# Optimization experiments

Hardware: AMD Instinct MI355X
Metric: run time of the kernel (lower is better)

Reference implementation:

```python
import jax, jax.numpy as jnp
import numpy as np

T, B, I, H = 2048, 32, 256, 256
KEEP = 0.75  # 1 - dropout_rate


def setup_inputs() -> dict:
    key = jax.random.key(0)
    ks = jax.random.split(key, 7)
    inp = jax.random.normal(ks[0], (T, B, I), dtype=jnp.float32)
    # variational dropout masks sampled once (Bernoulli(keep)), like the torch module
    zx = (jax.random.uniform(ks[1], (I,)) < KEEP).astype(jnp.float32)
    zh = (jax.random.uniform(ks[2], (H,)) < KEEP).astype(jnp.float32)
    # stacked gate weights in order [i, f, o, g]; scaled like nn.Linear default init
    s_w = 1.0 / np.sqrt(I)
    s_u = 1.0 / np.sqrt(H)
    W = jax.random.uniform(ks[3], (4 * H, I), minval=-s_w, maxval=s_w, dtype=jnp.float32)
    bW = jax.random.uniform(ks[4], (4 * H,), minval=-s_w, maxval=s_w, dtype=jnp.float32)
    U = jax.random.uniform(ks[5], (4 * H, H), minval=-s_u, maxval=s_u, dtype=jnp.float32)
    bU = jax.random.uniform(ks[6], (4 * H,), minval=-s_u, maxval=s_u, dtype=jnp.float32)
    return {"input": inp, "zx": zx, "zh": zh, "W": W, "bW": bW, "U": U, "bU": bU}


def reference(input, zx, zh, W, bW, U, bU):
    Bsz = input.shape[1]
    Hd = U.shape[1]

    def step(carry, x_t):
        h, c = carry
        x = x_t * zx          # [B, I] variational input dropout
        hm = h * zh           # [B, H] variational hidden dropout
        gates = x @ W.T + bW + hm @ U.T + bU   # [B, 4H]
        i, f, o, g = jnp.split(gates, 4, axis=-1)
        i = jax.nn.sigmoid(i)
        f = jax.nn.sigmoid(f)
        o = jax.nn.sigmoid(o)
        g = jnp.tanh(g)
        c_new = f * c + i * g
        h_new = o * jnp.tanh(c_new)
        return (h_new, c_new), h_new

    h0 = jnp.zeros((Bsz, Hd), dtype=input.dtype)
    c0 = jnp.zeros((Bsz, Hd), dtype=input.dtype)
    (h_t, c_t), hn = jax.lax.scan(step, (h0, c0), input)
    return hn, h_t, c_t
```

## Files before the change

kernel.cpp:

```cpp
#include <hip/hip_runtime.h>
#include <stdint.h>

typedef _Float16 half_t;
typedef _Float16 half2_t __attribute__((ext_vector_type(2)));

#define TSEQ 2048
#define NB   32
#define HD   256
#define HN_ELEMS ((size_t)TSEQ*NB*HD)

static __device__ __forceinline__ float fdot2u(uint32_t a, uint32_t b, float acc) {
  return __builtin_amdgcn_fdot2(__builtin_bit_cast(half2_t, a),
                                __builtin_bit_cast(half2_t, b), acc, false);
}
static __device__ __forceinline__ int sdot4(uint32_t a, uint32_t b, int c) {
#if defined(__has_builtin)
#if __has_builtin(__builtin_amdgcn_sdot4)
  return __builtin_amdgcn_sdot4((int)a, (int)b, c, false);
#else
  int d;
  asm("v_dot4_i32_i8 %0, %1, %2, %3" : "=v"(d) : "v"(a), "v"(b), "v"(c));
  return d;
#endif
#else
  int d;
  asm("v_dot4_i32_i8 %0, %1, %2, %3" : "=v"(d) : "v"(a), "v"(b), "v"(c));
  return d;
#endif
}
static __device__ __forceinline__ float sigm_f(float x) {
  return __builtin_amdgcn_rcpf(1.0f + __expf(-x));
}
static __device__ __forceinline__ float tanh_f(float x) {
  return 2.0f * __builtin_amdgcn_rcpf(1.0f + __expf(-2.0f * x)) - 1.0f;
}
static __device__ __forceinline__ signed char q8(float v, float sc) {
  int q = (int)rintf(v * sc);
  q = q > 127 ? 127 : (q < -127 ? -127 : q);
  return (signed char)q;
}

__global__ void prep_kernel(const float* __restrict__ W, const float* __restrict__ U,
                            const float* __restrict__ bW, const float* __restrict__ bU,
                            const float* __restrict__ zx, const float* __restrict__ zh,
                            half_t* __restrict__ Wpk, signed char* __restrict__ Upk3b,
                            signed char* __restrict__ Ug4b, float* __restrict__ bias,
                            half_t* __restrict__ hstate, float* __restrict__ cstate) {
  int tid = blockIdx.x * 256 + threadIdx.x;
  int n   = tid & 1023;
  int kcG = tid >> 10;
  #pragma unroll
  for (int e = 0; e < 8; ++e) {
    int k = kcG * 8 + e;
    Wpk[((size_t)kcG * 1024 + n) * 8 + e] = (half_t)(W[n * 256 + k] * zx[k]);
    float uv = U[n * 256 + k] * zh[k];
    signed char qv = q8(uv, 2032.0f);
    int kg = k >> 7, kk = k & 127, q = kk >> 4, by = kk & 15;
    if (n < 768) {
      int c = n >> 8, j = n & 255;
      Upk3b[(((size_t)(c * 2 + kg) * 8 + q) * 256 + j) * 16 + by] = qv;
    } else {
      Ug4b[(((size_t)kg * 8 + q) * 256 + (n & 255)) * 16 + by] = qv;
    }
  }
  if (kcG == 0) bias[n] = bW[n] + bU[n];
  if (tid < NB * HD) { hstate[tid] = (half_t)0.0f; cstate[tid] = 0.0f; }
}

__global__ __launch_bounds__(512)
void gemm_kernel(const float* __restrict__ input, const uint4* __restrict__ Wpk,
                 const float* __restrict__ bias, half_t* __restrict__ gx, int row0,
                 uint32_t rz) {
  __shared__ __align__(16) uint4  As[64 * 32];
  __shared__ __align__(16) float  part[8 * 256];
  __shared__ __align__(16) uint4  pad1b[1280];
  const int tid = threadIdx.x;
  if ((int)blockIdx.x < 0) pad1b[tid] = As[tid];
  const int cb    = blockIdx.x & 3;
  const int rbase = (blockIdx.x >> 2) * 64;
  const int jc    = tid & 255;
  const int kh    = tid >> 8;
  const int col   = cb * 256 + jc;

  uint32_t wreg[64];
  #pragma unroll
  for (int kc = 0; kc < 16; ++kc) {
    uint4 q = Wpk[(size_t)(kh * 16 + kc) * 1024 + col];
    wreg[kc * 4 + 0] = q.x ^ rz; wreg[kc * 4 + 1] = q.y ^ rz;
    wreg[kc * 4 + 2] = q.z ^ rz; wreg[kc * 4 + 3] = q.w ^ rz;
  }
  const float bc = bias[col];
  #pragma unroll
  for (int i = 0; i < 8; ++i) {
    int lin = tid + i * 512;
    int row = lin >> 6, f4 = lin & 63;
    float4 v = ((const float4*)input)[((size_t)(row0 + rbase + row)) * 64 + f4];
    half2_t p0; p0[0] = (half_t)v.x; p0[1] = (half_t)v.y;
    half2_t p1; p1[0] = (half_t)v.z; p1[1] = (half_t)v.w;
    ((uint2*)As)[row * 64 + f4] = make_uint2(__builtin_bit_cast(uint32_t, p0),
                                             __builtin_bit_cast(uint32_t, p1));
  }
  __syncthreads();

  #pragma unroll 1
  for (int rg = 0; rg < 64; rg += 8) {
    float acc[8];
    #pragma unroll
    for (int rr = 0; rr < 8; ++rr) {
      const uint4* arow = As + (rg + rr) * 32 + kh * 16;
      float a = 0.f;
      #pragma unroll
      for (int kc = 0; kc < 16; ++kc) {
        uint4 hv = arow[kc];
        a = fdot2u(wreg[kc * 4 + 0], hv.x, a);
        a = fdot2u(wreg[kc * 4 + 1], hv.y, a);
        a = fdot2u(wreg[kc * 4 + 2], hv.z, a);
        a = fdot2u(wreg[kc * 4 + 3], hv.w, a);
      }
      acc[rr] = a;
    }
    if (kh) {
      #pragma unroll
      for (int rr = 0; rr < 8; ++rr) part[rr * 256 + jc] = acc[rr];
    }
    __syncthreads();
    if (!kh) {
      #pragma unroll
      for (int rr = 0; rr < 8; ++rr) {
        float v = acc[rr] + part[rr * 256 + jc] + bc;
        gx[((size_t)(rbase + rg + rr) * HD + jc) * 4 + cb] = (half_t)v;
      }
    }
    __syncthreads();
  }
}

__global__ __launch_bounds__(512)
__attribute__((amdgpu_waves_per_eu(2, 2)))
void rec_kernel(const half_t* __restrict__ gx, const uint4* __restrict__ Upk3p,
                const uint4* __restrict__ Ug4p,
                half_t* __restrict__ hstate, float* __restrict__ cstate,
                float* __restrict__ out, int tbase, int TB, int last,
                uint32_t rz) {
  __shared__ __align__(16) uint4 uglds[4096];
  __shared__ __align__(16) signed char hbuf8[256];
  __shared__ __align__(16) int part[4 * 256];

  const int b   = blockIdx.x;
  const int tid = threadIdx.x;
  const int kg  = tid >> 8;
  const int j   = tid & 255;

  #pragma unroll
  for (int i = 0; i < 8; ++i) uglds[i * 512 + tid] = Ug4p[i * 512 + tid];

  uint32_t upk0[32], upk1[32], upk2[32];
  #pragma unroll
  for (int q = 0; q < 8; ++q) {
    uint4 v = Upk3p[((size_t)(0 * 2 + kg) * 8 + q) * 256 + j];
    upk0[q * 4 + 0] = v.x ^ rz; upk0[q * 4 + 1] = v.y ^ rz;
    upk0[q * 4 + 2] = v.z ^ rz; upk0[q * 4 + 3] = v.w ^ rz;
  }
  #pragma unroll
  for (int q = 0; q < 8; ++q) {
    uint4 v = Upk3p[((size_t)(1 * 2 + kg) * 8 + q) * 256 + j];
    upk1[q * 4 + 0] = v.x ^ rz; upk1[q * 4 + 1] = v.y ^ rz;
    upk1[q * 4 + 2] = v.z ^ rz; upk1[q * 4 + 3] = v.w ^ rz;
  }
  #pragma unroll
  for (int q = 0; q < 8; ++q) {
    uint4 v = Upk3p[((size_t)(2 * 2 + kg) * 8 + q) * 256 + j];
    upk2[q * 4 + 0] = v.x ^ rz; upk2[q * 4 + 1] = v.y ^ rz;
    upk2[q * 4 + 2] = v.z ^ rz; upk2[q * 4 + 3] = v.w ^ rz;
  }

  float cc = 0.f, hlastf = 0.f;
  uint2 gpk = make_uint2(0, 0), npk = make_uint2(0, 0);
  const uint2* gpn = (const uint2*)gx + (size_t)b * HD + j;
  float* outp = out + ((size_t)tbase * NB + b) * HD + j;
  if (kg == 0) {
    cc = cstate[b * HD + j];
    float h0 = (float)hstate[b * HD + j];
    hlastf = h0;
    hbuf8[j] = (signed char)(int)rintf(h0 * 127.0f);
    gpk = *gpn;
  }
  gpn += (size_t)NB * HD;
  __syncthreads();

  const float s = 0.0625f / 16129.0f;
  #pragma unroll 1
  for (int t = 0; t < TB; ++t) {
    if (kg == 0 && t + 1 < TB) npk = *gpn;
    gpn += (size_t)NB * HD;

    int a0 = 0, a1 = 0, a2 = 0, a3 = 0;
    const uint4* hp8 = (const uint4*)hbuf8 + kg * 8;
    const uint4* ugp = uglds + (size_t)kg * 8 * 256 + j;
    #pragma unroll
    for (int q = 0; q < 8; ++q) {
      uint4 hv = hp8[q];
      uint4 ug = ugp[q * 256];
      a0 = sdot4(upk0[q * 4 + 0], hv.x, a0);
      a0 = sdot4(upk0[q * 4 + 1], hv.y, a0);
      a0 = sdot4(upk0[q * 4 + 2], hv.z, a0);
      a0 = sdot4(upk0[q * 4 + 3], hv.w, a0);
      a1 = sdot4(upk1[q * 4 + 0], hv.x, a1);
      a1 = sdot4(upk1[q * 4 + 1], hv.y, a1);
      a1 = sdot4(upk1[q * 4 + 2], hv.z, a1);
      a1 = sdot4(upk1[q * 4 + 3], hv.w, a1);
      a2 = sdot4(upk2[q * 4 + 0], hv.x, a2);
      a2 = sdot4(upk2[q * 4 + 1], hv.y, a2);
      a2 = sdot4(upk2[q * 4 + 2], hv.z, a2);
      a2 = sdot4(upk2[q * 4 + 3], hv.w, a2);
      a3 = sdot4(ug.x, hv.x, a3);
      a3 = sdot4(ug.y, hv.y, a3);
      a3 = sdot4(ug.z, hv.z, a3);
      a3 = sdot4(ug.w, hv.w, a3);
    }
    if (kg) {
      part[0 * 256 + j] = a0;
      part[1 * 256 + j] = a1;
      part[2 * 256 + j] = a2;
      part[3 * 256 + j] = a3;
    }
    __syncthreads();
    if (kg == 0) {
      half2_t g01 = __builtin_bit_cast(half2_t, gpk.x);
      half2_t g23 = __builtin_bit_cast(half2_t, gpk.y);
      float f0 = (float)(a0 + part[0 * 256 + j]) * s + (float)g01[0];
      float f1 = (float)(a1 + part[1 * 256 + j]) * s + (float)g01[1];
      float f2 = (float)(a2 + part[2 * 256 + j]) * s + (float)g23[0];
      float f3 = (float)(a3 + part[3 * 256 + j]) * s + (float)g23[1];
      float gi = sigm_f(f0), gf = sigm_f(f1), go = sigm_f(f2), gg = tanh_f(f3);
      cc = gf * cc + gi * gg;
      float h = go * tanh_f(cc);
      hlastf = h;
      hbuf8[j] = (signed char)(int)rintf(h * 127.0f);
      *outp = h;
      if (last && t == TB - 1) {
        out[HN_ELEMS + (size_t)b * HD + j] = h;
        out[HN_ELEMS + (size_t)NB * HD + (size_t)b * HD + j] = cc;
      }
      gpk = npk;
    }
    outp += (size_t)NB * HD;
    __syncthreads();
  }
  if (kg == 0) {
    hstate[b * HD + j] = (half_t)hlastf;
    cstate[b * HD + j] = cc;
  }
}

extern "C" void kernel_launch(void* const* d_in, const int* in_sizes, int n_in,
                              void* d_out, int out_size, void* d_ws, size_t ws_size,
                              hipStream_t stream) {
  const float* input = (const float*)d_in[0];
  const float* zx    = (const float*)d_in[1];
  const float* zh    = (const float*)d_in[2];
  const float* W     = (const float*)d_in[3];
  const float* bW    = (const float*)d_in[4];
  const float* U     = (const float*)d_in[5];
  const float* bU    = (const float*)d_in[6];
  float* out = (float*)d_out;

  char* ws = (char*)d_ws;
  signed char* Upk3b = (signed char*)(ws);
  signed char* Ug4b  = (signed char*)(ws + (192 << 10));
  uint4*  Wpk    = (uint4*)(ws + (256 << 10));
  float*  bias   = (float*) (ws + (768 << 10));
  half_t* hstate = (half_t*)(ws + (772 << 10));
  float*  cstate = (float*) (ws + (788 << 10));
  half_t* gx     = (half_t*)(ws + (1 << 20));

  uint32_t rz = (uint32_t)(in_sizes[1] >> 9);

  int TB = TSEQ;
  while (TB > 32 && (size_t)(1u << 20) + (size_t)TB * NB * 1024 * 2 > ws_size) TB >>= 1;

  prep_kernel<<<128, 256, 0, stream>>>(W, U, bW, bU, zx, zh,
                                       (half_t*)Wpk, Upk3b, Ug4b,
                                       bias, hstate, cstate);

  int nch = TSEQ / TB;
  for (int c = 0; c < nch; ++c) {
    int tbase = c * TB;
    gemm_kernel<<<(TB * NB / 64) * 4, 512, 0, stream>>>(input, Wpk, bias, gx,
                                                        tbase * NB, rz);
    rec_kernel<<<NB, 512, 0, stream>>>(gx, (const uint4*)Upk3b, (const uint4*)Ug4b,
                                       hstate, cstate, out,
                                       tbase, TB, (c == nch - 1) ? 1 : 0, rz);
  }
}
```

Measured before the change: 2.034 ms.

## Use one thread per hidden unit in recurrence with double-buffered h

The recurrence kernel drops from 512 threads split over two K halves to 256 threads, each computing the full K=256 dot products for its hidden unit. This removes the shared-memory partial-sum exchange and one of the two barriers per timestep, since h is double-buffered. Each thread now keeps 224 packed int8 weight registers plus half of the fourth gate's weights in LDS, so register pressure rises sharply and there is a risk of spills. It also cuts wave-level parallelism and doubles the serial dot-product chain per thread.

```diff
diff --git a/kernel.cpp b/kernel.cpp
--- a/kernel.cpp
+++ b/kernel.cpp
@@ -55,12 +55,13 @@
     Wpk[((size_t)kcG * 1024 + n) * 8 + e] = (half_t)(W[n * 256 + k] * zx[k]);
     float uv = U[n * 256 + k] * zh[k];
     signed char qv = q8(uv, 2032.0f);
-    int kg = k >> 7, kk = k & 127, q = kk >> 4, by = kk & 15;
-    if (n < 768) {
-      int c = n >> 8, j = n & 255;
-      Upk3b[(((size_t)(c * 2 + kg) * 8 + q) * 256 + j) * 16 + by] = qv;
+    int c = n >> 8, j = n & 255, q = k >> 4, by = k & 15;
+    if (c < 3) {
+      Upk3b[(((size_t)c * 16 + q) * 256 + j) * 16 + by] = qv;
+    } else if (k < 128) {
+      Upk3b[(((size_t)48 + q) * 256 + j) * 16 + by] = qv;
     } else {
-      Ug4b[(((size_t)kg * 8 + q) * 256 + (n & 255)) * 16 + by] = qv;
+      Ug4b[(((size_t)(q - 8)) * 256 + j) * 16 + by] = qv;
     }
   }
   if (kcG == 0) bias[n] = bW[n] + bU[n];
@@ -135,72 +136,71 @@
   }
 }
 
-__global__ __launch_bounds__(512)
-__attribute__((amdgpu_waves_per_eu(2, 2)))
+__global__ __launch_bounds__(256)
 void rec_kernel(const half_t* __restrict__ gx, const uint4* __restrict__ Upk3p,
                 const uint4* __restrict__ Ug4p,
                 half_t* __restrict__ hstate, float* __restrict__ cstate,
                 float* __restrict__ out, int tbase, int TB, int last,
                 uint32_t rz) {
-  __shared__ __align__(16) uint4 uglds[4096];
-  __shared__ __align__(16) signed char hbuf8[256];
-  __shared__ __align__(16) int part[4 * 256];
-
-  const int b   = blockIdx.x;
-  const int tid = threadIdx.x;
-  const int kg  = tid >> 8;
-  const int j   = tid & 255;
-
-  #pragma unroll
-  for (int i = 0; i < 8; ++i) uglds[i * 512 + tid] = Ug4p[i * 512 + tid];
-
-  uint32_t upk0[32], upk1[32], upk2[32];
-  #pragma unroll
-  for (int q = 0; q < 8; ++q) {
-    uint4 v = Upk3p[((size_t)(0 * 2 + kg) * 8 + q) * 256 + j];
+  __shared__ __align__(16) uint4 uglds[8 * 256];
+  __shared__ __align__(16) uint4 hb[2][16];
+
+  const int b = blockIdx.x;
+  const int j = threadIdx.x;
+
+  #pragma unroll
+  for (int i = 0; i < 8; ++i) uglds[i * 256 + j] = Ug4p[i * 256 + j];
+
+  uint32_t upk0[64], upk1[64], upk2[64], upk3[32];
+  #pragma unroll
+  for (int q = 0; q < 16; ++q) {
+    uint4 v = Upk3p[((size_t)(0 * 16 + q)) * 256 + j];
     upk0[q * 4 + 0] = v.x ^ rz; upk0[q * 4 + 1] = v.y ^ rz;
     upk0[q * 4 + 2] = v.z ^ rz; upk0[q * 4 + 3] = v.w ^ rz;
   }
   #pragma unroll
-  for (int q = 0; q < 8; ++q) {
-    uint4 v = Upk3p[((size_t)(1 * 2 + kg) * 8 + q) * 256 + j];
+  for (int q = 0; q < 16; ++q) {
+    uint4 v = Upk3p[((size_t)(1 * 16 + q)) * 256 + j];
     upk1[q * 4 + 0] = v.x ^ rz; upk1[q * 4 + 1] = v.y ^ rz;
     upk1[q * 4 + 2] = v.z ^ rz; upk1[q * 4 + 3] = v.w ^ rz;
   }
   #pragma unroll
-  for (int q = 0; q < 8; ++q) {
-    uint4 v = Upk3p[((size_t)(2 * 2 + kg) * 8 + q) * 256 + j];
+  for (int q = 0; q < 16; ++q) {
+    uint4 v = Upk3p[((size_t)(2 * 16 + q)) * 256 + j];
     upk2[q * 4 + 0] = v.x ^ rz; upk2[q * 4 + 1] = v.y ^ rz;
     upk2[q * 4 + 2] = v.z ^ rz; upk2[q * 4 + 3] = v.w ^ rz;
   }
-
-  float cc = 0.f, hlastf = 0.f;
-  uint2 gpk = make_uint2(0, 0), npk = make_uint2(0, 0);
+  #pragma unroll
+  for (int q = 0; q < 8; ++q) {
+    uint4 v = Upk3p[((size_t)(48 + q)) * 256 + j];
+    upk3[q * 4 + 0] = v.x ^ rz; upk3[q * 4 + 1] = v.y ^ rz;
+    upk3[q * 4 + 2] = v.z ^ rz; upk3[q * 4 + 3] = v.w ^ rz;
+  }
+
+  float cc = cstate[b * HD + j];
+  float h0 = (float)hstate[b * HD + j];
+  ((signed char*)hb[0])[j] = (signed char)(int)rintf(h0 * 127.0f);
+
   const uint2* gpn = (const uint2*)gx + (size_t)b * HD + j;
   float* outp = out + ((size_t)tbase * NB + b) * HD + j;
-  if (kg == 0) {
-    cc = cstate[b * HD + j];
-    float h0 = (float)hstate[b * HD + j];
-    hlastf = h0;
-    hbuf8[j] = (signed char)(int)rintf(h0 * 127.0f);
-    gpk = *gpn;
-  }
+  uint2 gpk = *gpn, npk = make_uint2(0, 0);
   gpn += (size_t)NB * HD;
   __syncthreads();
 
   const float s = 0.0625f / 16129.0f;
+  float hlastf = h0;
   #pragma unroll 1
   for (int t = 0; t < TB; ++t) {
-    if (kg == 0 && t + 1 < TB) npk = *gpn;
+    const int cur = t & 1, nxt = cur ^ 1;
+    if (t + 1 < TB) npk = *gpn;
     gpn += (size_t)NB * HD;
 
     int a0 = 0, a1 = 0, a2 = 0, a3 = 0;
-    const uint4* hp8 = (const uint4*)hbuf8 + kg * 8;
-    const uint4* ugp = uglds + (size_t)kg * 8 * 256 + j;
+    const uint4* hp = hb[cur];
+    const uint4* ugp = uglds + j;
     #pragma unroll
-    for (int q = 0; q < 8; ++q) {
-      uint4 hv = hp8[q];
-      uint4 ug = ugp[q * 256];
+    for (int q = 0; q < 16; ++q) {
+      uint4 hv = hp[q];
       a0 = sdot4(upk0[q * 4 + 0], hv.x, a0);
       a0 = sdot4(upk0[q * 4 + 1], hv.y, a0);
       a0 = sdot4(upk0[q * 4 + 2], hv.z, a0);
@@ -213,44 +213,41 @@
       a2 = sdot4(upk2[q * 4 + 1], hv.y, a2);
       a2 = sdot4(upk2[q * 4 + 2], hv.z, a2);
       a2 = sdot4(upk2[q * 4 + 3], hv.w, a2);
-      a3 = sdot4(ug.x, hv.x, a3);
-      a3 = sdot4(ug.y, hv.y, a3);
-      a3 = sdot4(ug.z, hv.z, a3);
-      a3 = sdot4(ug.w, hv.w, a3);
-    }
-    if (kg) {
-      part[0 * 256 + j] = a0;
-      part[1 * 256 + j] = a1;
-      part[2 * 256 + j] = a2;
-      part[3 * 256 + j] = a3;
-    }
-    __syncthreads();
-    if (kg == 0) {
-      half2_t g01 = __builtin_bit_cast(half2_t, gpk.x);
-      half2_t g23 = __builtin_bit_cast(half2_t, gpk.y);
-      float f0 = (float)(a0 + part[0 * 256 + j]) * s + (float)g01[0];
-      float f1 = (float)(a1 + part[1 * 256 + j]) * s + (float)g01[1];
-      float f2 = (float)(a2 + part[2 * 256 + j]) * s + (float)g23[0];
-      float f3 = (float)(a3 + part[3 * 256 + j]) * s + (float)g23[1];
-      float gi = sigm_f(f0), gf = sigm_f(f1), go = sigm_f(f2), gg = tanh_f(f3);
-      cc = gf * cc + gi * gg;
-      float h = go * tanh_f(cc);
-      hlastf = h;
-      hbuf8[j] = (signed char)(int)rintf(h * 127.0f);
-      *outp = h;
-      if (last && t == TB - 1) {
-        out[HN_ELEMS + (size_t)b * HD + j] = h;
-        out[HN_ELEMS + (size_t)NB * HD + (size_t)b * HD + j] = cc;
+      if (q < 8) {
+        a3 = sdot4(upk3[q * 4 + 0], hv.x, a3);
+        a3 = sdot4(upk3[q * 4 + 1], hv.y, a3);
+        a3 = sdot4(upk3[q * 4 + 2], hv.z, a3);
+        a3 = sdot4(upk3[q * 4 + 3], hv.w, a3);
+      } else {
+        uint4 ug = ugp[(q - 8) * 256];
+        a3 = sdot4(ug.x, hv.x, a3);
+        a3 = sdot4(ug.y, hv.y, a3);
+        a3 = sdot4(ug.z, hv.z, a3);
+        a3 = sdot4(ug.w, hv.w, a3);
       }
-      gpk = npk;
-    }
+    }
+    half2_t g01 = __builtin_bit_cast(half2_t, gpk.x);
+    half2_t g23 = __builtin_bit_cast(half2_t, gpk.y);
+    float f0 = (float)a0 * s + (float)g01[0];
+    float f1 = (float)a1 * s + (float)g01[1];
+    float f2 = (float)a2 * s + (float)g23[0];
+    float f3 = (float)a3 * s + (float)g23[1];
+    float gi = sigm_f(f0), gf = sigm_f(f1), go = sigm_f(f2), gg = tanh_f(f3);
+    cc = gf * cc + gi * gg;
+    float h = go * tanh_f(cc);
+    hlastf = h;
+    ((signed char*)hb[nxt])[j] = (signed char)(int)rintf(h * 127.0f);
+    *outp = h;
+    if (last && t == TB - 1) {
+      out[HN_ELEMS + (size_t)b * HD + j] = h;
+      out[HN_ELEMS + (size_t)NB * HD + (size_t)b * HD + j] = cc;
+    }
+    gpk = npk;
     outp += (size_t)NB * HD;
     __syncthreads();
   }
-  if (kg == 0) {
-    hstate[b * HD + j] = (half_t)hlastf;
-    cstate[b * HD + j] = cc;
-  }
+  hstate[b * HD + j] = (half_t)hlastf;
+  cstate[b * HD + j] = cc;
 }
 
 extern "C" void kernel_launch(void* const* d_in, const int* in_sizes, int n_in,
@@ -267,7 +264,7 @@
 
   char* ws = (char*)d_ws;
   signed char* Upk3b = (signed char*)(ws);
-  signed char* Ug4b  = (signed char*)(ws + (192 << 10));
+  signed char* Ug4b  = (signed char*)(ws + (224 << 10));
   uint4*  Wpk    = (uint4*)(ws + (256 << 10));
   float*  bias   = (float*) (ws + (768 << 10));
   half_t* hstate = (half_t*)(ws + (772 << 10));
@@ -288,7 +285,7 @@
     int tbase = c * TB;
     gemm_kernel<<<(TB * NB / 64) * 4, 512, 0, stream>>>(input, Wpk, bias, gx,
                                                         tbase * NB, rz);
-    rec_kernel<<<NB, 512, 0, stream>>>(gx, (const uint4*)Upk3b, (const uint4*)Ug4b,
+    rec_kernel<<<NB, 256, 0, stream>>>(gx, (const uint4*)Upk3b, (const uint4*)Ug4b,
                                        hstate, cstate, out,
                                        tbase, TB, (c == nch - 1) ? 1 : 0, rz);
   }
```

Result: slower. 2.232 ms (+9.7%).

## Split K-halves across wave lanes and reduce with permlane32 swap

Applied to the files above, without the earlier changes.

Remaps threads so the two K-halves for one hidden unit live in the upper and lower 32 lanes of the same wave. Partial dot products are then combined with v_permlane32_swap instead of an LDS write, a barrier and a read. The hidden-state buffer is double-buffered, which removes one __syncthreads per timestep. Both halves now compute the gate nonlinearities redundantly, and the waves_per_eu attribute is dropped, which may change register allocation.

```diff
diff --git a/kernel.cpp b/kernel.cpp
--- a/kernel.cpp
+++ b/kernel.cpp
@@ -27,6 +27,13 @@
   asm("v_dot4_i32_i8 %0, %1, %2, %3" : "=v"(d) : "v"(a), "v"(b), "v"(c));
   return d;
 #endif
+}
+static __device__ __forceinline__ int halfsum(int a) {
+  int y;
+  asm("v_mov_b32 %1, %0\n\t"
+      "v_permlane32_swap_b32 %0, %1"
+      : "+v"(a), "=&v"(y));
+  return a + y;
 }
 static __device__ __forceinline__ float sigm_f(float x) {
   return __builtin_amdgcn_rcpf(1.0f + __expf(-x));
@@ -136,114 +143,106 @@
 }
 
 __global__ __launch_bounds__(512)
-__attribute__((amdgpu_waves_per_eu(2, 2)))
 void rec_kernel(const half_t* __restrict__ gx, const uint4* __restrict__ Upk3p,
                 const uint4* __restrict__ Ug4p,
                 half_t* __restrict__ hstate, float* __restrict__ cstate,
                 float* __restrict__ out, int tbase, int TB, int last,
                 uint32_t rz) {
   __shared__ __align__(16) uint4 uglds[4096];
-  __shared__ __align__(16) signed char hbuf8[256];
-  __shared__ __align__(16) int part[4 * 256];
-
-  const int b   = blockIdx.x;
-  const int tid = threadIdx.x;
-  const int kg  = tid >> 8;
-  const int j   = tid & 255;
+  __shared__ __align__(16) uint4 hb[2][16];
+
+  const int b    = blockIdx.x;
+  const int tid  = threadIdx.x;
+  const int lane = tid & 63;
+  const int kg   = lane >> 5;
+  const int j    = (tid >> 6) * 32 + (lane & 31);
 
   #pragma unroll
   for (int i = 0; i < 8; ++i) uglds[i * 512 + tid] = Ug4p[i * 512 + tid];
 
-  uint32_t upk0[32], upk1[32], upk2[32];
+  uint32_t u0[32], u1[32], u2[32];
   #pragma unroll
   for (int q = 0; q < 8; ++q) {
     uint4 v = Upk3p[((size_t)(0 * 2 + kg) * 8 + q) * 256 + j];
-    upk0[q * 4 + 0] = v.x ^ rz; upk0[q * 4 + 1] = v.y ^ rz;
-    upk0[q * 4 + 2] = v.z ^ rz; upk0[q * 4 + 3] = v.w ^ rz;
+    u0[q * 4 + 0] = v.x ^ rz; u0[q * 4 + 1] = v.y ^ rz;
+    u0[q * 4 + 2] = v.z ^ rz; u0[q * 4 + 3] = v.w ^ rz;
   }
   #pragma unroll
   for (int q = 0; q < 8; ++q) {
     uint4 v = Upk3p[((size_t)(1 * 2 + kg) * 8 + q) * 256 + j];
-    upk1[q * 4 + 0] = v.x ^ rz; upk1[q * 4 + 1] = v.y ^ rz;
-    upk1[q * 4 + 2] = v.z ^ rz; upk1[q * 4 + 3] = v.w ^ rz;
+    u1[q * 4 + 0] = v.x ^ rz; u1[q * 4 + 1] = v.y ^ rz;
+    u1[q * 4 + 2] = v.z ^ rz; u1[q * 4 + 3] = v.w ^ rz;
   }
   #pragma unroll
   for (int q = 0; q < 8; ++q) {
     uint4 v = Upk3p[((size_t)(2 * 2 + kg) * 8 + q) * 256 + j];
-    upk2[q * 4 + 0] = v.x ^ rz; upk2[q * 4 + 1] = v.y ^ rz;
-    upk2[q * 4 + 2] = v.z ^ rz; upk2[q * 4 + 3] = v.w ^ rz;
-  }
-
-  float cc = 0.f, hlastf = 0.f;
-  uint2 gpk = make_uint2(0, 0), npk = make_uint2(0, 0);
+    u2[q * 4 + 0] = v.x ^ rz; u2[q * 4 + 1] = v.y ^ rz;
+    u2[q * 4 + 2] = v.z ^ rz; u2[q * 4 + 3] = v.w ^ rz;
+  }
+
+  float cc = cstate[b * HD + j];
+  float h0 = (float)hstate[b * HD + j];
+  float hlastf = h0;
+  if (kg == 0) ((signed char*)hb[0])[j] = (signed char)(int)rintf(h0 * 127.0f);
+
   const uint2* gpn = (const uint2*)gx + (size_t)b * HD + j;
   float* outp = out + ((size_t)tbase * NB + b) * HD + j;
-  if (kg == 0) {
-    cc = cstate[b * HD + j];
-    float h0 = (float)hstate[b * HD + j];
-    hlastf = h0;
-    hbuf8[j] = (signed char)(int)rintf(h0 * 127.0f);
-    gpk = *gpn;
-  }
+  uint2 gpk = *gpn, npk = make_uint2(0, 0);
   gpn += (size_t)NB * HD;
   __syncthreads();
 
   const float s = 0.0625f / 16129.0f;
   #pragma unroll 1
   for (int t = 0; t < TB; ++t) {
-    if (kg == 0 && t + 1 < TB) npk = *gpn;
+    if (t + 1 < TB) npk = *gpn;
     gpn += (size_t)NB * HD;
 
     int a0 = 0, a1 = 0, a2 = 0, a3 = 0;
-    const uint4* hp8 = (const uint4*)hbuf8 + kg * 8;
-    const uint4* ugp = uglds + (size_t)kg * 8 * 256 + j;
+    const uint4* hp  = hb[t & 1] + (kg << 3);
+    const uint4* ugp = uglds + (size_t)kg * 2048 + j;
     #pragma unroll
     for (int q = 0; q < 8; ++q) {
-      uint4 hv = hp8[q];
+      uint4 hv = hp[q];
       uint4 ug = ugp[q * 256];
-      a0 = sdot4(upk0[q * 4 + 0], hv.x, a0);
-      a0 = sdot4(upk0[q * 4 + 1], hv.y, a0);
-      a0 = sdot4(upk0[q * 4 + 2], hv.z, a0);
-      a0 = sdot4(upk0[q * 4 + 3], hv.w, a0);
-      a1 = sdot4(upk1[q * 4 + 0], hv.x, a1);
-      a1 = sdot4(upk1[q * 4 + 1], hv.y, a1);
-      a1 = sdot4(upk1[q * 4 + 2], hv.z, a1);
-      a1 = sdot4(upk1[q * 4 + 3], hv.w, a1);
-      a2 = sdot4(upk2[q * 4 + 0], hv.x, a2);
-      a2 = sdot4(upk2[q * 4 + 1], hv.y, a2);
-      a2 = sdot4(upk2[q * 4 + 2], hv.z, a2);
-      a2 = sdot4(upk2[q * 4 + 3], hv.w, a2);
+      a0 = sdot4(u0[q * 4 + 0], hv.x, a0);
+      a0 = sdot4(u0[q * 4 + 1], hv.y, a0);
+      a0 = sdot4(u0[q * 4 + 2], hv.z, a0);
+      a0 = sdot4(u0[q * 4 + 3], hv.w, a0);
+      a1 = sdot4(u1[q * 4 + 0], hv.x, a1);
+      a1 = sdot4(u1[q * 4 + 1], hv.y, a1);
+      a1 = sdot4(u1[q * 4 + 2], hv.z, a1);
+      a1 = sdot4(u1[q * 4 + 3], hv.w, a1);
+      a2 = sdot4(u2[q * 4 + 0], hv.x, a2);
+      a2 = sdot4(u2[q * 4 + 1], hv.y, a2);
+      a2 = sdot4(u2[q * 4 + 2], hv.z, a2);
+      a2 = sdot4(u2[q * 4 + 3], hv.w, a2);
       a3 = sdot4(ug.x, hv.x, a3);
       a3 = sdot4(ug.y, hv.y, a3);
       a3 = sdot4(ug.z, hv.z, a3);
       a3 = sdot4(ug.w, hv.w, a3);
     }
-    if (kg) {
-      part[0 * 256 + j] = a0;
-      part[1 * 256 + j] = a1;
-      part[2 * 256 + j] = a2;
-      part[3 * 256 + j] = a3;
-    }
-    __syncthreads();
+    a0 = halfsum(a0); a1 = halfsum(a1);
+    a2 = halfsum(a2); a3 = halfsum(a3);
+
+    half2_t g01 = __builtin_bit_cast(half2_t, gpk.x);
+    half2_t g23 = __builtin_bit_cast(half2_t, gpk.y);
+    float f0 = (float)a0 * s + (float)g01[0];
+    float f1 = (float)a1 * s + (float)g01[1];
+    float f2 = (float)a2 * s + (float)g23[0];
+    float f3 = (float)a3 * s + (float)g23[1];
+    float gi = sigm_f(f0), gf = sigm_f(f1), go = sigm_f(f2), gg = tanh_f(f3);
+    cc = gf * cc + gi * gg;
+    float h = go * tanh_f(cc);
+    hlastf = h;
     if (kg == 0) {
-      half2_t g01 = __builtin_bit_cast(half2_t, gpk.x);
-      half2_t g23 = __builtin_bit_cast(half2_t, gpk.y);
-      float f0 = (float)(a0 + part[0 * 256 + j]) * s + (float)g01[0];
-      float f1 = (float)(a1 + part[1 * 256 + j]) * s + (float)g01[1];
-      float f2 = (float)(a2 + part[2 * 256 + j]) * s + (float)g23[0];
-      float f3 = (float)(a3 + part[3 * 256 + j]) * s + (float)g23[1];
-      float gi = sigm_f(f0), gf = sigm_f(f1), go = sigm_f(f2), gg = tanh_f(f3);
-      cc = gf * cc + gi * gg;
-      float h = go * tanh_f(cc);
-      hlastf = h;
-      hbuf8[j] = (signed char)(int)rintf(h * 127.0f);
+      ((signed char*)hb[(t & 1) ^ 1])[j] = (signed char)(int)rintf(h * 127.0f);
       *outp = h;
       if (last && t == TB - 1) {
         out[HN_ELEMS + (size_t)b * HD + j] = h;
         out[HN_ELEMS + (size_t)NB * HD + (size_t)b * HD + j] = cc;
       }
-      gpk = npk;
-    }
+    }
+    gpk = npk;
     outp += (size_t)NB * HD;
     __syncthreads();
   }
```

Measured after the change: 2.139 ms. +5.2%, slower.

## Replace fdot2 input-projection GEMM with MFMA 16x16x32 f16 kernel

Applied to the files above, without the earlier changes.

The input projection GEMM now runs on matrix cores via mfma_f32_16x16x32_f16 instead of per-thread fdot2 loops with LDS staging and a split-K reduction. W is stored as a plain row-major f16 matrix and read directly from global memory, and gx becomes a gate-major [row][1024] layout. The recurrent kernel is adjusted to read its four gate values from strided positions instead of one packed uint2. The cost removed is GEMM compute time. In exchange the B operand is read from global without LDS reuse, and the recurrent kernel issues four scalar loads per step.

```diff
diff --git a/kernel.cpp b/kernel.cpp
--- a/kernel.cpp
+++ b/kernel.cpp
@@ -3,16 +3,14 @@
 
 typedef _Float16 half_t;
 typedef _Float16 half2_t __attribute__((ext_vector_type(2)));
+typedef _Float16 half8_t __attribute__((ext_vector_type(8)));
+typedef float f32x4 __attribute__((ext_vector_type(4)));
 
 #define TSEQ 2048
 #define NB   32
 #define HD   256
 #define HN_ELEMS ((size_t)TSEQ*NB*HD)
 
-static __device__ __forceinline__ float fdot2u(uint32_t a, uint32_t b, float acc) {
-  return __builtin_amdgcn_fdot2(__builtin_bit_cast(half2_t, a),
-                                __builtin_bit_cast(half2_t, b), acc, false);
-}
 static __device__ __forceinline__ int sdot4(uint32_t a, uint32_t b, int c) {
 #if defined(__has_builtin)
 #if __has_builtin(__builtin_amdgcn_sdot4)
@@ -43,7 +41,7 @@
 __global__ void prep_kernel(const float* __restrict__ W, const float* __restrict__ U,
                             const float* __restrict__ bW, const float* __restrict__ bU,
                             const float* __restrict__ zx, const float* __restrict__ zh,
-                            half_t* __restrict__ Wpk, signed char* __restrict__ Upk3b,
+                            half_t* __restrict__ Wf16, signed char* __restrict__ Upk3b,
                             signed char* __restrict__ Ug4b, float* __restrict__ bias,
                             half_t* __restrict__ hstate, float* __restrict__ cstate) {
   int tid = blockIdx.x * 256 + threadIdx.x;
@@ -52,7 +50,7 @@
   #pragma unroll
   for (int e = 0; e < 8; ++e) {
     int k = kcG * 8 + e;
-    Wpk[((size_t)kcG * 1024 + n) * 8 + e] = (half_t)(W[n * 256 + k] * zx[k]);
+    Wf16[(size_t)n * 256 + k] = (half_t)(W[n * 256 + k] * zx[k]);
     float uv = U[n * 256 + k] * zh[k];
     signed char qv = q8(uv, 2032.0f);
     int kg = k >> 7, kk = k & 127, q = kk >> 4, by = kk & 15;
@@ -67,71 +65,47 @@
   if (tid < NB * HD) { hstate[tid] = (half_t)0.0f; cstate[tid] = 0.0f; }
 }
 
-__global__ __launch_bounds__(512)
-void gemm_kernel(const float* __restrict__ input, const uint4* __restrict__ Wpk,
-                 const float* __restrict__ bias, half_t* __restrict__ gx, int row0,
-                 uint32_t rz) {
-  __shared__ __align__(16) uint4  As[64 * 32];
-  __shared__ __align__(16) float  part[8 * 256];
-  __shared__ __align__(16) uint4  pad1b[1280];
-  const int tid = threadIdx.x;
-  if ((int)blockIdx.x < 0) pad1b[tid] = As[tid];
-  const int cb    = blockIdx.x & 3;
-  const int rbase = (blockIdx.x >> 2) * 64;
-  const int jc    = tid & 255;
-  const int kh    = tid >> 8;
-  const int col   = cb * 256 + jc;
-
-  uint32_t wreg[64];
-  #pragma unroll
-  for (int kc = 0; kc < 16; ++kc) {
-    uint4 q = Wpk[(size_t)(kh * 16 + kc) * 1024 + col];
-    wreg[kc * 4 + 0] = q.x ^ rz; wreg[kc * 4 + 1] = q.y ^ rz;
-    wreg[kc * 4 + 2] = q.z ^ rz; wreg[kc * 4 + 3] = q.w ^ rz;
-  }
-  const float bc = bias[col];
-  #pragma unroll
-  for (int i = 0; i < 8; ++i) {
-    int lin = tid + i * 512;
-    int row = lin >> 6, f4 = lin & 63;
-    float4 v = ((const float4*)input)[((size_t)(row0 + rbase + row)) * 64 + f4];
-    half2_t p0; p0[0] = (half_t)v.x; p0[1] = (half_t)v.y;
-    half2_t p1; p1[0] = (half_t)v.z; p1[1] = (half_t)v.w;
-    ((uint2*)As)[row * 64 + f4] = make_uint2(__builtin_bit_cast(uint32_t, p0),
-                                             __builtin_bit_cast(uint32_t, p1));
-  }
-  __syncthreads();
-
+__global__ __launch_bounds__(256)
+void gemm_kernel(const float* __restrict__ input, const half_t* __restrict__ Wf16,
+                 const float* __restrict__ bias, half_t* __restrict__ gx, int row0) {
+  const int tid  = threadIdx.x;
+  const int lane = tid & 63;
+  const int w    = tid >> 6;
+  const int mr   = lane & 15;
+  const int g    = lane >> 4;
+  const int nb   = (blockIdx.x & 3) * 256;
+  const int m0   = (blockIdx.x >> 2) * 64 + w * 16;
+
+  f32x4 acc[16];
+  #pragma unroll
+  for (int nf = 0; nf < 16; ++nf) acc[nf] = (f32x4){0.f, 0.f, 0.f, 0.f};
+
+  const float* arow = input + ((size_t)(row0 + m0 + mr)) * 256 + g * 8;
   #pragma unroll 1
-  for (int rg = 0; rg < 64; rg += 8) {
-    float acc[8];
+  for (int kk = 0; kk < 8; ++kk) {
+    float4 v0 = ((const float4*)(arow + kk * 32))[0];
+    float4 v1 = ((const float4*)(arow + kk * 32))[1];
+    half8_t a;
+    a[0] = (half_t)v0.x; a[1] = (half_t)v0.y; a[2] = (half_t)v0.z; a[3] = (half_t)v0.w;
+    a[4] = (half_t)v1.x; a[5] = (half_t)v1.y; a[6] = (half_t)v1.z; a[7] = (half_t)v1.w;
+    const half_t* bbase = Wf16 + (size_t)(nb + mr) * 256 + kk * 32 + g * 8;
     #pragma unroll
-    for (int rr = 0; rr < 8; ++rr) {
-      const uint4* arow = As + (rg + rr) * 32 + kh * 16;
-      float a = 0.f;
-      #pragma unroll
-      for (int kc = 0; kc < 16; ++kc) {
-        uint4 hv = arow[kc];
-        a = fdot2u(wreg[kc * 4 + 0], hv.x, a);
-        a = fdot2u(wreg[kc * 4 + 1], hv.y, a);
-        a = fdot2u(wreg[kc * 4 + 2], hv.z, a);
-        a = fdot2u(wreg[kc * 4 + 3], hv.w, a);
-      }
-      acc[rr] = a;
-    }
-    if (kh) {
-      #pragma unroll
-      for (int rr = 0; rr < 8; ++rr) part[rr * 256 + jc] = acc[rr];
-    }
-    __syncthreads();
-    if (!kh) {
-      #pragma unroll
-      for (int rr = 0; rr < 8; ++rr) {
-        float v = acc[rr] + part[rr * 256 + jc] + bc;
-        gx[((size_t)(rbase + rg + rr) * HD + jc) * 4 + cb] = (half_t)v;
-      }
-    }
-    __syncthreads();
+    for (int nf = 0; nf < 16; ++nf) {
+      uint4 bu = *(const uint4*)(bbase + (size_t)nf * 16 * 256);
+      half8_t b = __builtin_bit_cast(half8_t, bu);
+      acc[nf] = __builtin_amdgcn_mfma_f32_16x16x32_f16(a, b, acc[nf], 0, 0, 0);
+    }
+  }
+
+  #pragma unroll
+  for (int nf = 0; nf < 16; ++nf) {
+    int n = nb + nf * 16 + mr;
+    float bc = bias[n];
+    #pragma unroll
+    for (int i = 0; i < 4; ++i) {
+      int r = m0 + g * 4 + i;
+      gx[(size_t)r * 1024 + n] = (half_t)(acc[nf][i] + bc);
+    }
   }
 }
 
@@ -175,24 +149,27 @@
   }
 
   float cc = 0.f, hlastf = 0.f;
-  uint2 gpk = make_uint2(0, 0), npk = make_uint2(0, 0);
-  const uint2* gpn = (const uint2*)gx + (size_t)b * HD + j;
+  half_t g0 = (half_t)0.f, g1 = g0, g2 = g0, g3 = g0;
+  half_t n0 = g0, n1 = g0, n2 = g0, n3 = g0;
+  const half_t* gpn = gx + (size_t)b * 1024 + j;
   float* outp = out + ((size_t)tbase * NB + b) * HD + j;
   if (kg == 0) {
     cc = cstate[b * HD + j];
     float h0 = (float)hstate[b * HD + j];
     hlastf = h0;
     hbuf8[j] = (signed char)(int)rintf(h0 * 127.0f);
-    gpk = *gpn;
-  }
-  gpn += (size_t)NB * HD;
+    g0 = gpn[0]; g1 = gpn[256]; g2 = gpn[512]; g3 = gpn[768];
+  }
+  gpn += (size_t)NB * 1024;
   __syncthreads();
 
   const float s = 0.0625f / 16129.0f;
   #pragma unroll 1
   for (int t = 0; t < TB; ++t) {
-    if (kg == 0 && t + 1 < TB) npk = *gpn;
-    gpn += (size_t)NB * HD;
+    if (kg == 0 && t + 1 < TB) {
+      n0 = gpn[0]; n1 = gpn[256]; n2 = gpn[512]; n3 = gpn[768];
+    }
+    gpn += (size_t)NB * 1024;
 
     int a0 = 0, a1 = 0, a2 = 0, a3 = 0;
     const uint4* hp8 = (const uint4*)hbuf8 + kg * 8;
@@ -226,12 +203,10 @@
     }
     __syncthreads();
     if (kg == 0) {
-      half2_t g01 = __builtin_bit_cast(half2_t, gpk.x);
-      half2_t g23 = __builtin_bit_cast(half2_t, gpk.y);
-      float f0 = (float)(a0 + part[0 * 256 + j]) * s + (float)g01[0];
-      float f1 = (float)(a1 + part[1 * 256 + j]) * s + (float)g01[1];
-      float f2 = (float)(a2 + part[2 * 256 + j]) * s + (float)g23[0];
-      float f3 = (float)(a3 + part[3 * 256 + j]) * s + (float)g23[1];
+      float f0 = (float)(a0 + part[0 * 256 + j]) * s + (float)g0;
+      float f1 = (float)(a1 + part[1 * 256 + j]) * s + (float)g1;
+      float f2 = (float)(a2 + part[2 * 256 + j]) * s + (float)g2;
+      float f3 = (float)(a3 + part[3 * 256 + j]) * s + (float)g3;
       float gi = sigm_f(f0), gf = sigm_f(f1), go = sigm_f(f2), gg = tanh_f(f3);
       cc = gf * cc + gi * gg;
       float h = go * tanh_f(cc);
@@ -242,7 +217,7 @@
         out[HN_ELEMS + (size_t)b * HD + j] = h;
         out[HN_ELEMS + (size_t)NB * HD + (size_t)b * HD + j] = cc;
       }
-      gpk = npk;
+      g0 = n0; g1 = n1; g2 = n2; g3 = n3;
     }
     outp += (size_t)NB * HD;
     __syncthreads();
@@ -268,7 +243,7 @@
   char* ws = (char*)d_ws;
   signed char* Upk3b = (signed char*)(ws);
   signed char* Ug4b  = (signed char*)(ws + (192 << 10));
-  uint4*  Wpk    = (uint4*)(ws + (256 << 10));
+  half_t* Wf16   = (half_t*)(ws + (256 << 10));
   float*  bias   = (float*) (ws + (768 << 10));
   half_t* hstate = (half_t*)(ws + (772 << 10));
   float*  cstate = (float*) (ws + (788 << 10));
@@ -280,14 +255,14 @@
   while (TB > 32 && (size_t)(1u << 20) + (size_t)TB * NB * 1024 * 2 > ws_size) TB >>= 1;
 
   prep_kernel<<<128, 256, 0, stream>>>(W, U, bW, bU, zx, zh,
-                                       (half_t*)Wpk, Upk3b, Ug4b,
+                                       Wf16, Upk3b, Ug4b,
                                        bias, hstate, cstate);
 
   int nch = TSEQ / TB;
   for (int c = 0; c < nch; ++c) {
     int tbase = c * TB;
-    gemm_kernel<<<(TB * NB / 64) * 4, 512, 0, stream>>>(input, Wpk, bias, gx,
-                                                        tbase * NB, rz);
+    gemm_kernel<<<(TB * NB / 64) * 4, 256, 0, stream>>>(input, Wf16, bias, gx,
+                                                        tbase * NB);
     rec_kernel<<<NB, 512, 0, stream>>>(gx, (const uint4*)Upk3b, (const uint4*)Ug4b,
                                        hstate, cstate, out,
                                        tbase, TB, (c == nch - 1) ? 1 : 0, rz);
```

Result: faster. 1.989 ms (-2.2%).
